# Kernel tuning notes

Hardware: AMD Instinct MI355X
Metric: run time of the kernel (lower is better)

## Reference

```python
import jax, jax.numpy as jnp
import numpy as np

THRESH = 0.3
EPS = 1e-8
M = 256
D = 768


def setup_inputs() -> dict:
    key = jax.random.key(0)
    kx, kb, ka, kn = jax.random.split(key, 4)
    x = jax.random.normal(kx, (1, D), dtype=jnp.float32)
    base = jax.random.normal(kb, (M, D), dtype=jnp.float32)
    # correlate memories with x so that a realistic fraction passes the 0.3 cosine threshold
    alpha = jax.random.uniform(ka, (M,), minval=0.0, maxval=0.8)
    mem = alpha[:, None] * x[0][None, :] + jnp.sqrt(1.0 - alpha**2)[:, None] * base
    # pre-sampled injection noise (original: torch.randn * 0.1 per W element)
    noise = 0.1 * jax.random.normal(kn, (M, M, D), dtype=jnp.float32)
    return {"x": x, "mem": mem, "noise": noise}


def reference(x, mem, noise):
    # x: [1, D] query embedding; mem: [M, D] memory bank (k == memory embeddings)
    d = x.shape[-1]
    xv = x[0]                                   # [D]
    nx = jnp.maximum(jnp.linalg.norm(xv), EPS)
    nm = jnp.linalg.norm(mem, axis=-1)          # [M]
    nm_s = jnp.maximum(nm, EPS)
    Sx = xv.sum()
    Sm = mem.sum(-1)                            # [M]

    kx_dot = mem @ xv                           # [M] dot(k_i, x)
    mx_cos = kx_dot / (nm_s * nx)               # [M] cos(x, m_j) == cos(k_i, x)
    mask = (mx_cos > THRESH).astype(x.dtype)    # active memories A
    cnt = mask.sum()

    km_dot = mem @ mem.T                        # [M, M] dot(k_i, m_j)
    km_cos = km_dot / (nm_s[:, None] * nm_s[None, :])

    # c[a, i] = cos(k_i, m_a) + cos(k_i, x)  (scalar added to all D dims of k_i)
    c = km_cos.T + mx_cos[None, :]              # [M, M]

    # ||k'_{a,i}||^2 = ||k_i||^2 + 2 c sum(k_i) + D c^2
    nkp = jnp.sqrt(jnp.maximum(nm[None, :]**2 + 2.0 * c * Sm[None, :] + d * c**2, EPS**2))

    # cos(k'_{a,i}, x) = (dot(k_i,x) + c*sum(x)) / (||k'|| * ||x||)
    cos_kp_x = (kx_dot[None, :] + c * Sx) / (nkp * nx)

    # mean over a' in A of cos(k'_{a,i}, m_{a'}) in closed form
    A1 = (km_dot * (mask / nm_s)[None, :]).sum(-1)   # [M] (i-indexed)
    A2 = ((mask * Sm) / nm_s).sum()                  # scalar
    denom = nkp * jnp.maximum(cnt, 1.0)
    mean_cos_km = jnp.where(cnt > 0, (A1[None, :] + c * A2) / denom, 0.0)

    # W_{a,i} = k'_{a,i} + mean sim to x + mean sim to active mems; then noise; O_prev = 0
    W = mem[None, :, :] + (c + cos_kp_x + mean_cos_km)[:, :, None]   # [M, M, D]
    out = (W + noise) * mask[:, None, None]     # zero rows for inactive memories
    return out
```

## Files before the change

### kernel.cpp

```cpp
#include <hip/hip_runtime.h>
#include <hip/hip_bf16.h>
#include <math.h>

#define M 256
#define D 768
#define D4 (D/4)
#define THRESH 0.3
#define EPS 1e-8

typedef float vfloat4 __attribute__((ext_vector_type(4)));

#define WS_SM    0
#define WS_NM2   256
#define WS_KX    512
#define WS_NMS   768
#define WS_MX    1024
#define WS_W     1280
#define WS_MASK  1536
#define WS_SX    1792
#define WS_NX2   1793
#define WS_NX    1794
#define WS_CNT   1795
#define WS_A2    1796
#define WS_MEMT  2048
#define WS_ST    (2048 + D * M)

__global__ void k1_stats_transpose(const float* __restrict__ x,
                                   const float* __restrict__ mem,
                                   float* __restrict__ ws) {
    const int r = blockIdx.x;
    const int t = threadIdx.x;
    const float* row = (r < M) ? (mem + (size_t)r * D) : x;

    double s = 0.0, sq = 0.0, dt = 0.0;
    for (int d = t; d < D; d += 256) {
        float mf = row[d];
        double m = (double)mf;
        double xv = (double)x[d];
        s += m; sq += m * m; dt += m * xv;
        if (r < M) ws[WS_MEMT + d * M + r] = mf;
    }
    __shared__ double sh0[256], sh1[256], sh2[256];
    sh0[t] = s; sh1[t] = sq; sh2[t] = dt;
    __syncthreads();
    for (int k = 128; k > 0; k >>= 1) {
        if (t < k) { sh0[t] += sh0[t + k]; sh1[t] += sh1[t + k]; sh2[t] += sh2[t + k]; }
        __syncthreads();
    }
    if (t == 0) {
        if (r < M) {
            ws[WS_SM + r]  = (float)sh0[0];
            ws[WS_NM2 + r] = (float)sh1[0];
            ws[WS_KX + r]  = (float)sh2[0];
        } else {
            ws[WS_SX]  = (float)sh0[0];
            ws[WS_NX2] = (float)sh1[0];
        }
    }
}

__global__ void k2_derived(float* __restrict__ ws) {
    const int i = threadIdx.x;
    double nx = sqrt(fmax((double)ws[WS_NX2], 0.0));
    nx = fmax(nx, EPS);
    double nm2 = (double)ws[WS_NM2 + i];
    double nm  = sqrt(fmax(nm2, 0.0));
    double nms = fmax(nm, EPS);
    double mx  = (double)ws[WS_KX + i] / (nms * nx);
    double mask = (mx > THRESH) ? 1.0 : 0.0;

    ws[WS_NMS + i]  = (float)nms;
    ws[WS_MX + i]   = (float)mx;
    ws[WS_W + i]    = (float)(mask / nms);
    ws[WS_MASK + i] = (float)mask;

    __shared__ double shc[256], sha[256];
    shc[i] = mask;
    sha[i] = mask * (double)ws[WS_SM + i] / nms;
    __syncthreads();
    for (int k = 128; k > 0; k >>= 1) {
        if (i < k) { shc[i] += shc[i + k]; sha[i] += sha[i + k]; }
        __syncthreads();
    }
    if (i == 0) {
        ws[WS_NX]  = (float)nx;
        ws[WS_CNT] = (float)shc[0];
        ws[WS_A2]  = (float)sha[0];
    }
}

__global__ __launch_bounds__(256) void k3_s(const float* __restrict__ mem,
                                            float* __restrict__ ws) {
    const int i = blockIdx.x;
    const int a = threadIdx.x;

    __shared__ float lrow[D];
    for (int d = a; d < D; d += 256) lrow[d] = mem[(size_t)i * D + d];
    __syncthreads();

    const float* memT = ws + WS_MEMT;
    float acc0 = 0.f, acc1 = 0.f, acc2 = 0.f, acc3 = 0.f;
    #pragma unroll 4
    for (int d = 0; d < D; d += 4) {
        acc0 += memT[(d + 0) * M + a] * lrow[d + 0];
        acc1 += memT[(d + 1) * M + a] * lrow[d + 1];
        acc2 += memT[(d + 2) * M + a] * lrow[d + 2];
        acc3 += memT[(d + 3) * M + a] * lrow[d + 3];
    }
    const double g = (double)((acc0 + acc1) + (acc2 + acc3));

    __shared__ double shr[256];
    shr[a] = (double)ws[WS_W + a] * g;
    __syncthreads();
    for (int k = 128; k > 0; k >>= 1) {
        if (a < k) shr[a] += shr[a + k];
        __syncthreads();
    }
    const double A1 = shr[0];

    const double nmsi = (double)ws[WS_NMS + i];
    const double nm2  = (double)ws[WS_NM2 + i];
    const double Sm   = (double)ws[WS_SM + i];
    const double kx   = (double)ws[WS_KX + i];
    const double mxi  = (double)ws[WS_MX + i];
    const double nx   = (double)ws[WS_NX];
    const double Sx   = (double)ws[WS_SX];
    const double cnt  = (double)ws[WS_CNT];
    const double A2   = (double)ws[WS_A2];

    const double nmsa = (double)ws[WS_NMS + a];
    const double c = g / (nmsa * nmsi) + mxi;

    const double nkp = sqrt(fmax(nm2 + 2.0 * c * Sm + (double)D * c * c, EPS * EPS));
    const double cos_kp_x = (kx + c * Sx) / (nkp * nx);
    const double mean_cos_km = (cnt > 0.0) ? (A1 + c * A2) / (nkp * fmax(cnt, 1.0)) : 0.0;

    ws[WS_ST + i * M + a] = (float)(c + cos_kp_x + mean_cos_km);
}

__global__ __launch_bounds__(D4) void k4_final(const float* __restrict__ mem,
                                               const float* __restrict__ noise,
                                               const float* __restrict__ ws,
                                               float* __restrict__ out) {
    const int i = blockIdx.x;
    const int a = blockIdx.y;
    const int t = threadIdx.x;
    const size_t idx = ((size_t)(a * M + i)) * D4 + t;

    vfloat4 o;
    if (ws[WS_MASK + a] != 0.0f) {
        const float s = ws[WS_ST + i * M + a];
        vfloat4 m = ((const vfloat4*)mem)[(size_t)i * D4 + t];
        vfloat4 n = __builtin_nontemporal_load((const vfloat4*)noise + idx);
        o.x = m.x + s + n.x;
        o.y = m.y + s + n.y;
        o.z = m.z + s + n.z;
        o.w = m.w + s + n.w;
    } else {
        o = (vfloat4){0.f, 0.f, 0.f, 0.f};
    }
    __builtin_nontemporal_store(o, (vfloat4*)out + idx);
}

extern "C" void kernel_launch(void* const* d_in, const int* in_sizes, int n_in,
                              void* d_out, int out_size, void* d_ws, size_t ws_size,
                              hipStream_t stream) {
    const float* x     = (const float*)d_in[0];
    const float* mem   = (const float*)d_in[1];
    const float* noise = (const float*)d_in[2];
    float* out = (float*)d_out;
    float* ws  = (float*)d_ws;

    k1_stats_transpose<<<dim3(M + 1), dim3(256), 0, stream>>>(x, mem, ws);
    k2_derived<<<dim3(1), dim3(256), 0, stream>>>(ws);
    k3_s<<<dim3(M), dim3(256), 0, stream>>>(mem, ws);
    k4_final<<<dim3(M, M), dim3(D4), 0, stream>>>(mem, noise, ws, out);
}
```

Measured before the change: 338.3 us.

## Fuse derived-stats kernel into k3, vectorize memT layout, coarsen final kernel

Removes the single-block k2 launch by recomputing norms, mask, count and A2 redundantly inside every k3 block. It stores the transposed memory bank in a 4-interleaved layout so k3 can read vfloat4. The final streaming kernel now has each block handle 32 rows of i for one a, loading the scale factors once into shared memory, which cuts the block count by 32x. The cost is lower parallelism in the bandwidth-bound final kernel and extra redundant reduction work in k3.

New measurement: 345.8 us. 1.02x slower.

```diff
diff --git a/kernel.cpp b/kernel.cpp
--- a/kernel.cpp
+++ b/kernel.cpp
@@ -13,21 +13,15 @@
 #define WS_SM    0
 #define WS_NM2   256
 #define WS_KX    512
-#define WS_NMS   768
-#define WS_MX    1024
-#define WS_W     1280
-#define WS_MASK  1536
-#define WS_SX    1792
-#define WS_NX2   1793
-#define WS_NX    1794
-#define WS_CNT   1795
-#define WS_A2    1796
+#define WS_MASK  768
+#define WS_SX    1024
+#define WS_NX2   1025
 #define WS_MEMT  2048
 #define WS_ST    (2048 + D * M)
 
-__global__ void k1_stats_transpose(const float* __restrict__ x,
-                                   const float* __restrict__ mem,
-                                   float* __restrict__ ws) {
+__global__ __launch_bounds__(256) void k1_stats_transpose(const float* __restrict__ x,
+                                                          const float* __restrict__ mem,
+                                                          float* __restrict__ ws) {
     const int r = blockIdx.x;
     const int t = threadIdx.x;
     const float* row = (r < M) ? (mem + (size_t)r * D) : x;
@@ -38,7 +32,7 @@
         double m = (double)mf;
         double xv = (double)x[d];
         s += m; sq += m * m; dt += m * xv;
-        if (r < M) ws[WS_MEMT + d * M + r] = mf;
+        if (r < M) ws[WS_MEMT + (d >> 2) * (M * 4) + r * 4 + (d & 3)] = mf;
     }
     __shared__ double sh0[256], sh1[256], sh2[256];
     sh0[t] = s; sh1[t] = sq; sh2[t] = dt;
@@ -59,80 +53,62 @@
     }
 }
 
-__global__ void k2_derived(float* __restrict__ ws) {
-    const int i = threadIdx.x;
-    double nx = sqrt(fmax((double)ws[WS_NX2], 0.0));
-    nx = fmax(nx, EPS);
-    double nm2 = (double)ws[WS_NM2 + i];
-    double nm  = sqrt(fmax(nm2, 0.0));
-    double nms = fmax(nm, EPS);
-    double mx  = (double)ws[WS_KX + i] / (nms * nx);
-    double mask = (mx > THRESH) ? 1.0 : 0.0;
-
-    ws[WS_NMS + i]  = (float)nms;
-    ws[WS_MX + i]   = (float)mx;
-    ws[WS_W + i]    = (float)(mask / nms);
-    ws[WS_MASK + i] = (float)mask;
-
-    __shared__ double shc[256], sha[256];
-    shc[i] = mask;
-    sha[i] = mask * (double)ws[WS_SM + i] / nms;
-    __syncthreads();
-    for (int k = 128; k > 0; k >>= 1) {
-        if (i < k) { shc[i] += shc[i + k]; sha[i] += sha[i + k]; }
-        __syncthreads();
-    }
-    if (i == 0) {
-        ws[WS_NX]  = (float)nx;
-        ws[WS_CNT] = (float)shc[0];
-        ws[WS_A2]  = (float)sha[0];
-    }
-}
-
 __global__ __launch_bounds__(256) void k3_s(const float* __restrict__ mem,
                                             float* __restrict__ ws) {
     const int i = blockIdx.x;
     const int a = threadIdx.x;
 
-    __shared__ float lrow[D];
-    for (int d = a; d < D; d += 256) lrow[d] = mem[(size_t)i * D + d];
+    const double nx   = fmax(sqrt(fmax((double)ws[WS_NX2], 0.0)), EPS);
+    const double Sx   = (double)ws[WS_SX];
+    const double Sm_a = (double)ws[WS_SM + a];
+    const double nm2a = (double)ws[WS_NM2 + a];
+    const double kx_a = (double)ws[WS_KX + a];
+    const double nmsa = fmax(sqrt(fmax(nm2a, 0.0)), EPS);
+    const double mx_a = kx_a / (nmsa * nx);
+    const double maska = (mx_a > THRESH) ? 1.0 : 0.0;
+    const double w_a = maska / nmsa;
+    ws[WS_MASK + a] = (float)maska;
+
+    __shared__ vfloat4 lrow4[D4];
+    if (a < D4) lrow4[a] = ((const vfloat4*)mem)[(size_t)i * D4 + a];
     __syncthreads();
 
-    const float* memT = ws + WS_MEMT;
+    const vfloat4* memT4 = (const vfloat4*)(ws + WS_MEMT);
     float acc0 = 0.f, acc1 = 0.f, acc2 = 0.f, acc3 = 0.f;
-    #pragma unroll 4
-    for (int d = 0; d < D; d += 4) {
-        acc0 += memT[(d + 0) * M + a] * lrow[d + 0];
-        acc1 += memT[(d + 1) * M + a] * lrow[d + 1];
-        acc2 += memT[(d + 2) * M + a] * lrow[d + 2];
-        acc3 += memT[(d + 3) * M + a] * lrow[d + 3];
+    for (int dq = 0; dq < D4; dq += 4) {
+        vfloat4 v0 = memT4[(dq + 0) * M + a]; vfloat4 l0 = lrow4[dq + 0];
+        vfloat4 v1 = memT4[(dq + 1) * M + a]; vfloat4 l1 = lrow4[dq + 1];
+        vfloat4 v2 = memT4[(dq + 2) * M + a]; vfloat4 l2 = lrow4[dq + 2];
+        vfloat4 v3 = memT4[(dq + 3) * M + a]; vfloat4 l3 = lrow4[dq + 3];
+        acc0 += v0.x * l0.x + v0.y * l0.y + v0.z * l0.z + v0.w * l0.w;
+        acc1 += v1.x * l1.x + v1.y * l1.y + v1.z * l1.z + v1.w * l1.w;
+        acc2 += v2.x * l2.x + v2.y * l2.y + v2.z * l2.z + v2.w * l2.w;
+        acc3 += v3.x * l3.x + v3.y * l3.y + v3.z * l3.z + v3.w * l3.w;
     }
     const double g = (double)((acc0 + acc1) + (acc2 + acc3));
 
-    __shared__ double shr[256];
-    shr[a] = (double)ws[WS_W + a] * g;
+    __shared__ double shc[256], sha[256], shr[256];
+    shc[a] = maska;
+    sha[a] = maska * Sm_a / nmsa;
+    shr[a] = w_a * g;
     __syncthreads();
     for (int k = 128; k > 0; k >>= 1) {
-        if (a < k) shr[a] += shr[a + k];
+        if (a < k) { shc[a] += shc[a + k]; sha[a] += sha[a + k]; shr[a] += shr[a + k]; }
         __syncthreads();
     }
-    const double A1 = shr[0];
+    const double cnt = shc[0];
+    const double A2  = sha[0];
+    const double A1  = shr[0];
 
-    const double nmsi = (double)ws[WS_NMS + i];
-    const double nm2  = (double)ws[WS_NM2 + i];
-    const double Sm   = (double)ws[WS_SM + i];
-    const double kx   = (double)ws[WS_KX + i];
-    const double mxi  = (double)ws[WS_MX + i];
-    const double nx   = (double)ws[WS_NX];
-    const double Sx   = (double)ws[WS_SX];
-    const double cnt  = (double)ws[WS_CNT];
-    const double A2   = (double)ws[WS_A2];
+    const double nm2i = (double)ws[WS_NM2 + i];
+    const double Smi  = (double)ws[WS_SM + i];
+    const double kxi  = (double)ws[WS_KX + i];
+    const double nmsi = fmax(sqrt(fmax(nm2i, 0.0)), EPS);
+    const double mxi  = kxi / (nmsi * nx);
 
-    const double nmsa = (double)ws[WS_NMS + a];
     const double c = g / (nmsa * nmsi) + mxi;
-
-    const double nkp = sqrt(fmax(nm2 + 2.0 * c * Sm + (double)D * c * c, EPS * EPS));
-    const double cos_kp_x = (kx + c * Sx) / (nkp * nx);
+    const double nkp = sqrt(fmax(nm2i + 2.0 * c * Smi + (double)D * c * c, EPS * EPS));
+    const double cos_kp_x = (kxi + c * Sx) / (nkp * nx);
     const double mean_cos_km = (cnt > 0.0) ? (A1 + c * A2) / (nkp * fmax(cnt, 1.0)) : 0.0;
 
     ws[WS_ST + i * M + a] = (float)(c + cos_kp_x + mean_cos_km);
@@ -142,24 +118,37 @@
                                                const float* __restrict__ noise,
                                                const float* __restrict__ ws,
                                                float* __restrict__ out) {
-    const int i = blockIdx.x;
-    const int a = blockIdx.y;
-    const int t = threadIdx.x;
-    const size_t idx = ((size_t)(a * M + i)) * D4 + t;
+    const int a  = blockIdx.y;
+    const int i0 = blockIdx.x * 32;
+    const int t  = threadIdx.x;
 
-    vfloat4 o;
+    const vfloat4* mem4   = (const vfloat4*)mem;
+    const vfloat4* noise4 = (const vfloat4*)noise;
+    vfloat4* out4         = (vfloat4*)out;
+    const size_t base = ((size_t)a * M + i0) * D4 + t;
+
     if (ws[WS_MASK + a] != 0.0f) {
-        const float s = ws[WS_ST + i * M + a];
-        vfloat4 m = ((const vfloat4*)mem)[(size_t)i * D4 + t];
-        vfloat4 n = __builtin_nontemporal_load((const vfloat4*)noise + idx);
-        o.x = m.x + s + n.x;
-        o.y = m.y + s + n.y;
-        o.z = m.z + s + n.z;
-        o.w = m.w + s + n.w;
+        __shared__ float ssh[32];
+        if (t < 32) ssh[t] = ws[WS_ST + (i0 + t) * M + a];
+        __syncthreads();
+        #pragma unroll 4
+        for (int il = 0; il < 32; ++il) {
+            const float s = ssh[il];
+            vfloat4 m = mem4[(size_t)(i0 + il) * D4 + t];
+            vfloat4 n = __builtin_nontemporal_load(noise4 + base + (size_t)il * D4);
+            vfloat4 o;
+            o.x = m.x + s + n.x;
+            o.y = m.y + s + n.y;
+            o.z = m.z + s + n.z;
+            o.w = m.w + s + n.w;
+            __builtin_nontemporal_store(o, out4 + base + (size_t)il * D4);
+        }
     } else {
-        o = (vfloat4){0.f, 0.f, 0.f, 0.f};
+        const vfloat4 z = (vfloat4){0.f, 0.f, 0.f, 0.f};
+        #pragma unroll 8
+        for (int il = 0; il < 32; ++il)
+            __builtin_nontemporal_store(z, out4 + base + (size_t)il * D4);
     }
-    __builtin_nontemporal_store(o, (vfloat4*)out + idx);
 }
 
 extern "C" void kernel_launch(void* const* d_in, const int* in_sizes, int n_in,
@@ -172,7 +161,6 @@
     float* ws  = (float*)d_ws;
 
     k1_stats_transpose<<<dim3(M + 1), dim3(256), 0, stream>>>(x, mem, ws);
-    k2_derived<<<dim3(1), dim3(256), 0, stream>>>(ws);
     k3_s<<<dim3(M), dim3(256), 0, stream>>>(mem, ws);
-    k4_final<<<dim3(M, M), dim3(D4), 0, stream>>>(mem, noise, ws, out);
+    k4_final<<<dim3(8, M), dim3(D4), 0, stream>>>(mem, noise, ws, out);
 }
```
